# Kernel optimization log

Measured on AMD Instinct MI355X. Metric: run time of the kernel, lower is better.

Reference implementation:

```python
import jax, jax.numpy as jnp
import numpy as np

NEG_SLOPE = 0.2  # PyG GATConv LeakyReLU slope
N_NODES = 50000
N_EDGES = 800000
F_IN, HID, HEADS, N_CLS = 166, 64, 8, 2


def setup_inputs() -> dict:
    key = jax.random.key(0)
    ks = jax.random.split(key, 16)
    s = 0.1
    return {
        "x": jax.random.normal(ks[0], (N_NODES, F_IN), jnp.float32),
        "edge_index": jax.random.randint(ks[1], (2, N_EDGES), 0, N_NODES, jnp.int64),
        "W1": jax.random.normal(ks[2], (F_IN, HEADS * HID), jnp.float32) * s,
        "a_src1": jax.random.normal(ks[3], (HEADS, HID), jnp.float32) * s,
        "a_dst1": jax.random.normal(ks[4], (HEADS, HID), jnp.float32) * s,
        "b1": jnp.zeros((HEADS * HID,), jnp.float32),
        # conv_final: 512 -> 64, 1 head, mean (concat=False)
        "W2": jax.random.normal(ks[5], (HEADS * HID, HID), jnp.float32) * s,
        "a_src2": jax.random.normal(ks[6], (1, HID), jnp.float32) * s,
        "a_dst2": jax.random.normal(ks[7], (1, HID), jnp.float32) * s,
        "b2": jnp.zeros((HID,), jnp.float32),
        # classifier MLP 64 -> 64 -> 2
        "Wc1": jax.random.normal(ks[8], (HID, HID), jnp.float32) * s,
        "bc1": jnp.zeros((HID,), jnp.float32),
        "Wc2": jax.random.normal(ks[9], (HID, N_CLS), jnp.float32) * s,
        "bc2": jnp.zeros((N_CLS,), jnp.float32),
    }


def gat_layer(x, src, dst, W, a_src, a_dst, b, concat):
    """PyG-style GATConv (eval mode, self-loops already in src/dst)."""
    N = x.shape[0]
    H, C = a_src.shape
    xp = (x @ W).reshape(N, H, C)                 # [N,H,C] projected features
    al_src = jnp.sum(xp * a_src, axis=-1)         # [N,H]
    al_dst = jnp.sum(xp * a_dst, axis=-1)         # [N,H]
    e = jax.nn.leaky_relu(al_src[src] + al_dst[dst], NEG_SLOPE)  # [E,H]
    # segment softmax over incoming edges of each target node
    m = jax.ops.segment_max(e, dst, num_segments=N)
    ex = jnp.exp(e - m[dst])
    denom = jax.ops.segment_sum(ex, dst, num_segments=N)
    alpha = ex / denom[dst]                       # [E,H]
    out = jax.ops.segment_sum(alpha[:, :, None] * xp[src], dst, num_segments=N)  # [N,H,C]
    out = out.reshape(N, H * C) if concat else out.mean(axis=1)
    return out + b


def reference(x, edge_index, W1, a_src1, a_dst1, b1, W2, a_src2, a_dst2, b2, Wc1, bc1, Wc2, bc2):
    N = x.shape[0]
    loops = jnp.arange(N, dtype=edge_index.dtype)
    src = jnp.concatenate([edge_index[0], loops])  # add self-loops (PyG default)
    dst = jnp.concatenate([edge_index[1], loops])
    h = jax.nn.elu(gat_layer(x, src, dst, W1, a_src1, a_dst1, b1, concat=True))
    h = gat_layer(h, src, dst, W2, a_src2, a_dst2, b2, concat=False)
    h = jax.nn.relu(h @ Wc1 + bc1)
    return h @ Wc2 + bc2
```

## Files before the change

kernel.cpp:

```cpp
#include <hip/hip_runtime.h>

#define NN   50000
#define E0   800000
#define ET   850000
#define FIN  166
#define KP1  192
#define HID  64
#define NH   8
#define F1   512
#define SCHUNK 52
#define DEGPAD (1024*SCHUNK)

typedef __attribute__((ext_vector_type(8))) short short8;
typedef __attribute__((ext_vector_type(4))) float f32x4;
typedef __attribute__((ext_vector_type(4))) int int4v;
typedef unsigned short ush;

__device__ __forceinline__ float bf2f(unsigned short u){
  unsigned int x = ((unsigned int)u) << 16;
  return __builtin_bit_cast(float, x);
}
__device__ __forceinline__ unsigned short f2bf(float f){
  unsigned int x = __builtin_bit_cast(unsigned int, f);
  x += 0x7FFFu + ((x >> 16) & 1u);
  return (unsigned short)(x >> 16);
}

__global__ __launch_bounds__(256) void k_prep_all(const float* __restrict__ x,
                                                  const float* __restrict__ W1,
                                                  const float* __restrict__ W2,
                                                  const int* __restrict__ ei,
                                                  ush* __restrict__ xpad,
                                                  ush* __restrict__ W1t,
                                                  ush* __restrict__ W2t,
                                                  int* __restrict__ deg){
  const int T0 = NN*KP1;
  const int T1 = T0 + 512*KP1;
  const int T2 = T1 + HID*F1;
  const int T3 = T2 + ET;
  int i = blockIdx.x*256 + threadIdx.x;
  if (i >= T3) return;
  if (i < T0){
    int n = i / KP1, k = i % KP1;
    xpad[i] = f2bf(k < FIN ? x[(size_t)n*FIN + k] : 0.f);
  } else if (i < T1){
    int j = i - T0; int col = j / KP1, k = j % KP1;
    W1t[j] = f2bf(k < FIN ? W1[(size_t)k*512 + col] : 0.f);
  } else if (i < T2){
    int j = i - T1; int col = j / F1, k = j % F1;
    W2t[j] = f2bf(W2[(size_t)k*HID + col]);
  } else {
    int e = i - T2;
    int dst = (e < E0) ? ei[E0 + e] : (e - E0);
    atomicAdd(&deg[dst], 1);
  }
}

__global__ __launch_bounds__(1024) void k_scan(const int* __restrict__ deg,
                                               int* __restrict__ offs){
  __shared__ int sums[1024];
  int t = threadIdx.x;
  int base = t * SCHUNK;
  int4v v[13];
  int loc = 0;
  #pragma unroll
  for (int c = 0; c < 13; c++){
    v[c] = *(const int4v*)(deg + base + c*4);
    loc += v[c].x + v[c].y + v[c].z + v[c].w;
  }
  sums[t] = loc; __syncthreads();
  for (int off = 1; off < 1024; off <<= 1){
    int s = (t >= off) ? sums[t - off] : 0;
    __syncthreads();
    sums[t] += s;
    __syncthreads();
  }
  int run = sums[t] - loc;
  #pragma unroll
  for (int c = 0; c < 13; c++){
    int i0 = base + c*4;
    if (i0 + 0 < NN) offs[i0 + 0] = run;  run += v[c].x;
    if (i0 + 1 < NN) offs[i0 + 1] = run;  run += v[c].y;
    if (i0 + 2 < NN) offs[i0 + 2] = run;  run += v[c].z;
    if (i0 + 3 < NN) offs[i0 + 3] = run;  run += v[c].w;
  }
  if (t == 1023) offs[NN] = sums[1023];
}

__global__ __launch_bounds__(256) void k_scatter(const int* __restrict__ ei,
                                                 const int* __restrict__ offs,
                                                 int* __restrict__ cur,
                                                 int* __restrict__ esrc){
  for (int e = blockIdx.x*256 + threadIdx.x; e < ET; e += gridDim.x*256){
    int src, dst;
    if (e < E0){ src = ei[e]; dst = ei[E0 + e]; }
    else       { src = e - E0; dst = src; }
    int pos = offs[dst] + atomicAdd(&cur[dst], 1);
    esrc[pos] = src;
  }
}

__global__ __launch_bounds__(256) void k_gemm1(const ush* __restrict__ xpad,
                                               const ush* __restrict__ W1t,
                                               const float* __restrict__ a_s,
                                               const float* __restrict__ a_d,
                                               ush* __restrict__ xp1,
                                               float* __restrict__ als,
                                               float* __restrict__ ald){
  __shared__ ush As[128][40];
  __shared__ ush Bs[128][40];
  const int m0 = blockIdx.x*128, n0 = blockIdx.y*128;
  const int t = threadIdx.x, wid = t>>6, l = t&63;
  const int wr = wid>>1, wc = wid&1;
  const int lr = l&15, ksl = (l>>4)*8;
  const int srow = t>>1, sc = (t&1)*16;

  f32x4 acc[4][4];
  #pragma unroll
  for (int m = 0; m < 4; m++)
    #pragma unroll
    for (int n = 0; n < 4; n++)
      #pragma unroll
      for (int j = 0; j < 4; j++) acc[m][n][j] = 0.f;

  const int gr = m0 + srow;
  const ush* Ap = xpad + (size_t)gr*KP1 + sc;
  const ush* Bp = W1t + (size_t)(n0 + srow)*KP1 + sc;

  for (int s = 0; s < 6; s++){
    const int kk = s*32;
    short8 a0, a1;
    #pragma unroll
    for (int j = 0; j < 8; j++){ a0[j] = 0; a1[j] = 0; }
    if (gr < NN){ a0 = *(const short8*)(Ap + kk); a1 = *(const short8*)(Ap + kk + 8); }
    short8 b0 = *(const short8*)(Bp + kk);
    short8 b1 = *(const short8*)(Bp + kk + 8);
    *(short8*)&As[srow][sc]   = a0;
    *(short8*)&As[srow][sc+8] = a1;
    *(short8*)&Bs[srow][sc]   = b0;
    *(short8*)&Bs[srow][sc+8] = b1;
    __syncthreads();
    short8 af[4], bfr[4];
    #pragma unroll
    for (int m = 0; m < 4; m++) af[m]  = *(const short8*)&As[wr*64 + m*16 + lr][ksl];
    #pragma unroll
    for (int n = 0; n < 4; n++) bfr[n] = *(const short8*)&Bs[wc*64 + n*16 + lr][ksl];
    #pragma unroll
    for (int m = 0; m < 4; m++)
      #pragma unroll
      for (int n = 0; n < 4; n++)
        acc[m][n] = __builtin_amdgcn_mfma_f32_16x16x32_bf16(af[m], bfr[n], acc[m][n], 0, 0, 0);
    __syncthreads();
  }

  #pragma unroll
  for (int m = 0; m < 4; m++)
    #pragma unroll
    for (int n = 0; n < 4; n++)
      #pragma unroll
      for (int j = 0; j < 4; j++){
        int row = m0 + wr*64 + m*16 + (l>>4)*4 + j;
        int col = n0 + wc*64 + n*16 + lr;
        if (row < NN) xp1[(size_t)row*F1 + col] = f2bf(acc[m][n][j]);
      }

  const int head = blockIdx.y*2 + wc;
  float asv[4], adv[4];
  #pragma unroll
  for (int n = 0; n < 4; n++){
    asv[n] = a_s[head*64 + n*16 + lr];
    adv[n] = a_d[head*64 + n*16 + lr];
  }
  #pragma unroll
  for (int m = 0; m < 4; m++)
    #pragma unroll
    for (int j = 0; j < 4; j++){
      float ps = 0.f, pd = 0.f;
      #pragma unroll
      for (int n = 0; n < 4; n++){
        ps = fmaf(acc[m][n][j], asv[n], ps);
        pd = fmaf(acc[m][n][j], adv[n], pd);
      }
      #pragma unroll
      for (int o = 1; o < 16; o <<= 1){
        ps += __shfl_xor(ps, o, 64);
        pd += __shfl_xor(pd, o, 64);
      }
      if (lr == 0){
        int row = m0 + wr*64 + m*16 + (l>>4)*4 + j;
        if (row < NN){
          als[(size_t)row*NH + head] = fminf(fmaxf(ps, -30.f), 30.f);
          ald[(size_t)row*NH + head] = fminf(fmaxf(pd, -30.f), 30.f);
        }
      }
    }
}

__global__ __launch_bounds__(256) void k_gemm2(const ush* __restrict__ h1,
                                               const ush* __restrict__ W2t,
                                               const float* __restrict__ a_s,
                                               const float* __restrict__ a_d,
                                               ush* __restrict__ xp2,
                                               float* __restrict__ als,
                                               float* __restrict__ ald){
  __shared__ ush As[128][40];
  __shared__ ush Bs[64][40];
  const int m0 = blockIdx.x*128;
  const int t = threadIdx.x, wid = t>>6, l = t&63;
  const int lr = l&15, ksl = (l>>4)*8;
  const int srow = t>>1, sc = (t&1)*16;

  f32x4 acc[2][4];
  #pragma unroll
  for (int m = 0; m < 2; m++)
    #pragma unroll
    for (int n = 0; n < 4; n++)
      #pragma unroll
      for (int j = 0; j < 4; j++) acc[m][n][j] = 0.f;

  const int gr = m0 + srow;
  const ush* Ap = h1 + (size_t)gr*F1 + sc;
  const ush* Bp = W2t + (size_t)srow*F1 + sc;

  for (int s = 0; s < 16; s++){
    const int kk = s*32;
    short8 a0, a1;
    #pragma unroll
    for (int j = 0; j < 8; j++){ a0[j] = 0; a1[j] = 0; }
    if (gr < NN){ a0 = *(const short8*)(Ap + kk); a1 = *(const short8*)(Ap + kk + 8); }
    *(short8*)&As[srow][sc]   = a0;
    *(short8*)&As[srow][sc+8] = a1;
    if (t < 128){
      short8 b0 = *(const short8*)(Bp + kk);
      short8 b1 = *(const short8*)(Bp + kk + 8);
      *(short8*)&Bs[srow][sc]   = b0;
      *(short8*)&Bs[srow][sc+8] = b1;
    }
    __syncthreads();
    short8 af[2], bfr[4];
    #pragma unroll
    for (int m = 0; m < 2; m++) af[m]  = *(const short8*)&As[wid*32 + m*16 + lr][ksl];
    #pragma unroll
    for (int n = 0; n < 4; n++) bfr[n] = *(const short8*)&Bs[n*16 + lr][ksl];
    #pragma unroll
    for (int m = 0; m < 2; m++)
      #pragma unroll
      for (int n = 0; n < 4; n++)
        acc[m][n] = __builtin_amdgcn_mfma_f32_16x16x32_bf16(af[m], bfr[n], acc[m][n], 0, 0, 0);
    __syncthreads();
  }

  #pragma unroll
  for (int m = 0; m < 2; m++)
    #pragma unroll
    for (int n = 0; n < 4; n++)
      #pragma unroll
      for (int j = 0; j < 4; j++){
        int row = m0 + wid*32 + m*16 + (l>>4)*4 + j;
        int col = n*16 + lr;
        if (row < NN) xp2[(size_t)row*HID + col] = f2bf(acc[m][n][j]);
      }

  float asv[4], adv[4];
  #pragma unroll
  for (int n = 0; n < 4; n++){
    asv[n] = a_s[n*16 + lr];
    adv[n] = a_d[n*16 + lr];
  }
  #pragma unroll
  for (int m = 0; m < 2; m++)
    #pragma unroll
    for (int j = 0; j < 4; j++){
      float ps = 0.f, pd = 0.f;
      #pragma unroll
      for (int n = 0; n < 4; n++){
        ps = fmaf(acc[m][n][j], asv[n], ps);
        pd = fmaf(acc[m][n][j], adv[n], pd);
      }
      #pragma unroll
      for (int o = 1; o < 16; o <<= 1){
        ps += __shfl_xor(ps, o, 64);
        pd += __shfl_xor(pd, o, 64);
      }
      if (lr == 0){
        int row = m0 + wid*32 + m*16 + (l>>4)*4 + j;
        if (row < NN){
          als[row] = fminf(fmaxf(ps, -30.f), 30.f);
          ald[row] = fminf(fmaxf(pd, -30.f), 30.f);
        }
      }
    }
}

__global__ __launch_bounds__(256) void k_agg1(const int* __restrict__ offs,
                                              const int* __restrict__ esrc,
                                              const ush* __restrict__ xp1,
                                              const float* __restrict__ als,
                                              const float* __restrict__ ald,
                                              const float* __restrict__ b1,
                                              ush* __restrict__ h1){
  int w = (blockIdx.x*256 + threadIdx.x) >> 6;
  int l = threadIdx.x & 63;
  if (w >= NN) return;
  int h = l >> 3;
  int f0 = l * 8;
  float ad = ald[w*NH + h];
  int s0 = offs[w], s1 = offs[w+1];
  float accA[8], accB[8];
  #pragma unroll
  for (int j = 0; j < 8; j++){ accA[j] = 0.f; accB[j] = 0.f; }
  float den = 0.f;

  for (int base = s0; base < s1; base += 64){
    int cnt = min(64, s1 - base);
    int myE = (base + l < s1) ? esrc[base + l] : 0;
    int j = 0;
    for (; j + 4 <= cnt; j += 4){
      int sA = __shfl(myE, j,   64);
      int sB = __shfl(myE, j+1, 64);
      int sC = __shfl(myE, j+2, 64);
      int sD = __shfl(myE, j+3, 64);
      float eA = als[sA*NH + h] + ad;
      float eB = als[sB*NH + h] + ad;
      float eC = als[sC*NH + h] + ad;
      float eD = als[sD*NH + h] + ad;
      eA = fmaxf(eA, 0.2f*eA); eB = fmaxf(eB, 0.2f*eB);
      eC = fmaxf(eC, 0.2f*eC); eD = fmaxf(eD, 0.2f*eD);
      float wA = __expf(eA), wB = __expf(eB), wC = __expf(eC), wD = __expf(eD);
      short8 vA = *(const short8*)(xp1 + (size_t)sA*F1 + f0);
      short8 vB = *(const short8*)(xp1 + (size_t)sB*F1 + f0);
      short8 vC = *(const short8*)(xp1 + (size_t)sC*F1 + f0);
      short8 vD = *(const short8*)(xp1 + (size_t)sD*F1 + f0);
      den += (wA + wB) + (wC + wD);
      #pragma unroll
      for (int jj = 0; jj < 8; jj++){
        accA[jj] = fmaf(wA, bf2f((ush)vA[jj]), accA[jj]);
        accB[jj] = fmaf(wB, bf2f((ush)vB[jj]), accB[jj]);
        accA[jj] = fmaf(wC, bf2f((ush)vC[jj]), accA[jj]);
        accB[jj] = fmaf(wD, bf2f((ush)vD[jj]), accB[jj]);
      }
    }
    for (; j < cnt; j++){
      int sA = __shfl(myE, j, 64);
      float eA = als[sA*NH + h] + ad;
      eA = fmaxf(eA, 0.2f*eA);
      float wA = __expf(eA);
      short8 vA = *(const short8*)(xp1 + (size_t)sA*F1 + f0);
      den += wA;
      #pragma unroll
      for (int jj = 0; jj < 8; jj++)
        accA[jj] = fmaf(wA, bf2f((ush)vA[jj]), accA[jj]);
    }
  }
  float inv = 1.f / den;
  #pragma unroll
  for (int jj = 0; jj < 8; jj++){
    float o = (accA[jj] + accB[jj])*inv + b1[f0 + jj];
    o = o > 0.f ? o : expm1f(o);
    h1[(size_t)w*F1 + f0 + jj] = f2bf(o);
  }
}

__global__ __launch_bounds__(256) void k_agg2(const int* __restrict__ offs,
                                              const int* __restrict__ esrc,
                                              const ush* __restrict__ xp2,
                                              const float* __restrict__ als,
                                              const float* __restrict__ ald,
                                              const float* __restrict__ b2,
                                              const float* __restrict__ Wc1,
                                              const float* __restrict__ bc1,
                                              const float* __restrict__ Wc2,
                                              const float* __restrict__ bc2,
                                              float* __restrict__ out){
  int w = (blockIdx.x*256 + threadIdx.x) >> 6;
  int l = threadIdx.x & 63;
  if (w >= NN) return;
  float ad = ald[w];
  int s0 = offs[w], s1 = offs[w+1];
  float accA = 0.f, accB = 0.f, den = 0.f;

  for (int base = s0; base < s1; base += 64){
    int cnt = min(64, s1 - base);
    int myE = (base + l < s1) ? esrc[base + l] : 0;
    int j = 0;
    for (; j + 4 <= cnt; j += 4){
      int sA = __shfl(myE, j,   64);
      int sB = __shfl(myE, j+1, 64);
      int sC = __shfl(myE, j+2, 64);
      int sD = __shfl(myE, j+3, 64);
      float eA = als[sA] + ad, eB = als[sB] + ad, eC = als[sC] + ad, eD = als[sD] + ad;
      eA = fmaxf(eA, 0.2f*eA); eB = fmaxf(eB, 0.2f*eB);
      eC = fmaxf(eC, 0.2f*eC); eD = fmaxf(eD, 0.2f*eD);
      float wA = __expf(eA), wB = __expf(eB), wC = __expf(eC), wD = __expf(eD);
      float xA = bf2f(xp2[(size_t)sA*HID + l]);
      float xB = bf2f(xp2[(size_t)sB*HID + l]);
      float xC = bf2f(xp2[(size_t)sC*HID + l]);
      float xD = bf2f(xp2[(size_t)sD*HID + l]);
      den += (wA + wB) + (wC + wD);
      accA = fmaf(wA, xA, accA); accB = fmaf(wB, xB, accB);
      accA = fmaf(wC, xC, accA); accB = fmaf(wD, xD, accB);
    }
    for (; j < cnt; j++){
      int sA = __shfl(myE, j, 64);
      float eA = als[sA] + ad;
      eA = fmaxf(eA, 0.2f*eA);
      float wA = __expf(eA);
      den += wA;
      accA = fmaf(wA, bf2f(xp2[(size_t)sA*HID + l]), accA);
    }
  }
  float h2 = (accA + accB) / den + b2[l];
  float r = 0.f;
  #pragma unroll
  for (int k = 0; k < 64; k++){
    float hk = __shfl(h2, k, 64);
    r = fmaf(hk, Wc1[k*HID + l], r);
  }
  r += bc1[l];
  r = fmaxf(r, 0.f);
  float p0 = r * Wc2[l*2 + 0];
  float p1 = r * Wc2[l*2 + 1];
  #pragma unroll
  for (int o = 1; o < 64; o <<= 1){
    p0 += __shfl_xor(p0, o, 64);
    p1 += __shfl_xor(p1, o, 64);
  }
  if (l == 0){
    out[(size_t)w*2 + 0] = p0 + bc2[0];
    out[(size_t)w*2 + 1] = p1 + bc2[1];
  }
}

extern "C" void kernel_launch(void* const* d_in, const int* in_sizes, int n_in,
                              void* d_out, int out_size, void* d_ws, size_t ws_size,
                              hipStream_t stream){
  const float* x   = (const float*)d_in[0];
  const int*   ei  = (const int*)  d_in[1];
  const float* W1  = (const float*)d_in[2];
  const float* as1 = (const float*)d_in[3];
  const float* ad1 = (const float*)d_in[4];
  const float* b1  = (const float*)d_in[5];
  const float* W2  = (const float*)d_in[6];
  const float* as2 = (const float*)d_in[7];
  const float* ad2 = (const float*)d_in[8];
  const float* b2  = (const float*)d_in[9];
  const float* Wc1 = (const float*)d_in[10];
  const float* bc1 = (const float*)d_in[11];
  const float* Wc2 = (const float*)d_in[12];
  const float* bc2 = (const float*)d_in[13];
  float* out = (float*)d_out;

  char* p = (char*)d_ws; size_t off = 0;
  auto alloc = [&](size_t b){ void* r = p + off; off = (off + b + 255) & ~(size_t)255; return r; };
  ush* xpad = (ush*)alloc((size_t)NN*KP1*2);
  ush* W1t  = (ush*)alloc((size_t)512*KP1*2);
  ush* W2t  = (ush*)alloc((size_t)HID*F1*2);
  ush* xp1  = (ush*)alloc((size_t)NN*F1*2);
  ush* h1   = (ush*)alloc((size_t)NN*F1*2);
  ush* xp2  = (ush*)alloc((size_t)NN*HID*2);
  float* als1 = (float*)alloc((size_t)NN*NH*4);
  float* ald1 = (float*)alloc((size_t)NN*NH*4);
  float* als2 = (float*)alloc((size_t)NN*4);
  float* ald2 = (float*)alloc((size_t)NN*4);
  int* deg  = (int*)alloc((size_t)DEGPAD*4);
  int* cur  = (int*)alloc((size_t)NN*4);
  int* offs = (int*)alloc((size_t)(NN+1)*4);
  int* esrc = (int*)alloc((size_t)ET*4);

  hipMemsetAsync(deg, 0, (size_t)DEGPAD*4, stream);
  hipMemsetAsync(cur, 0, (size_t)NN*4, stream);

  const int T3 = NN*KP1 + 512*KP1 + HID*F1 + ET;
  k_prep_all<<<(T3 + 255)/256, 256, 0, stream>>>(x, W1, W2, ei, xpad, W1t, W2t, deg);
  k_scan<<<1, 1024, 0, stream>>>(deg, offs);
  k_scatter<<<(ET + 255)/256, 256, 0, stream>>>(ei, offs, cur, esrc);

  k_gemm1<<<dim3(391, 4), 256, 0, stream>>>(xpad, W1t, as1, ad1, xp1, als1, ald1);
  k_agg1<<<12500, 256, 0, stream>>>(offs, esrc, xp1, als1, ald1, b1, h1);

  k_gemm2<<<391, 256, 0, stream>>>(h1, W2t, as2, ad2, xp2, als2, ald2);
  k_agg2<<<12500, 256, 0, stream>>>(offs, esrc, xp2, als2, ald2, b2, Wc1, bc1, Wc2, bc2, out);
}
```

Baseline: 394.0 us.

## Precompute per-edge attention weights in separate kernels before aggregation

Adds a destination array to the CSR scatter and two new edge-wise kernels that compute leaky-relu and exp attention weights per edge (and per head) into workspace buffers. The aggregation kernels then read these weights from contiguous CSR-ordered memory instead of gathering als by source and running exp inline. The change removes random als gathers and exp work from the gather-bound aggregation loops. In exchange it adds two kernel launches and extra global traffic, about 27 MB written and read for layer 1 weights, plus an edst array. It also splits the first aggregation into two half-node launches.

```diff
diff --git a/kernel.cpp b/kernel.cpp
--- a/kernel.cpp
+++ b/kernel.cpp
@@ -90,13 +90,15 @@
 __global__ __launch_bounds__(256) void k_scatter(const int* __restrict__ ei,
                                                  const int* __restrict__ offs,
                                                  int* __restrict__ cur,
-                                                 int* __restrict__ esrc){
+                                                 int* __restrict__ esrc,
+                                                 int* __restrict__ edst){
   for (int e = blockIdx.x*256 + threadIdx.x; e < ET; e += gridDim.x*256){
     int src, dst;
     if (e < E0){ src = ei[e]; dst = ei[E0 + e]; }
     else       { src = e - E0; dst = src; }
     int pos = offs[dst] + atomicAdd(&cur[dst], 1);
     esrc[pos] = src;
+    edst[pos] = dst;
   }
 }
 
@@ -292,19 +294,45 @@
     }
 }
 
+__global__ __launch_bounds__(256) void k_ew1(const int* __restrict__ esrc,
+                                             const int* __restrict__ edst,
+                                             const float* __restrict__ als,
+                                             const float* __restrict__ ald,
+                                             float* __restrict__ wt1){
+  int i = blockIdx.x*256 + threadIdx.x;
+  if (i >= ET*NH) return;
+  int pos = i >> 3, h = i & 7;
+  int src = esrc[pos], dst = edst[pos];
+  float v = als[src*NH + h] + ald[dst*NH + h];
+  v = fmaxf(v, 0.2f*v);
+  wt1[i] = __expf(v);
+}
+
+__global__ __launch_bounds__(256) void k_ew2(const int* __restrict__ esrc,
+                                             const int* __restrict__ edst,
+                                             const float* __restrict__ als,
+                                             const float* __restrict__ ald,
+                                             float* __restrict__ wt2){
+  int pos = blockIdx.x*256 + threadIdx.x;
+  if (pos >= ET) return;
+  float v = als[esrc[pos]] + ald[edst[pos]];
+  v = fmaxf(v, 0.2f*v);
+  wt2[pos] = __expf(v);
+}
+
 __global__ __launch_bounds__(256) void k_agg1(const int* __restrict__ offs,
                                               const int* __restrict__ esrc,
                                               const ush* __restrict__ xp1,
-                                              const float* __restrict__ als,
-                                              const float* __restrict__ ald,
+                                              const float* __restrict__ wt1,
                                               const float* __restrict__ b1,
-                                              ush* __restrict__ h1){
+                                              ush* __restrict__ h1,
+                                              int nodeBase, int nodeCnt){
   int w = (blockIdx.x*256 + threadIdx.x) >> 6;
   int l = threadIdx.x & 63;
-  if (w >= NN) return;
+  if (w >= nodeCnt) return;
+  w += nodeBase;
   int h = l >> 3;
   int f0 = l * 8;
-  float ad = ald[w*NH + h];
   int s0 = offs[w], s1 = offs[w+1];
   float accA[8], accB[8];
   #pragma unroll
@@ -320,13 +348,10 @@
       int sB = __shfl(myE, j+1, 64);
       int sC = __shfl(myE, j+2, 64);
       int sD = __shfl(myE, j+3, 64);
-      float eA = als[sA*NH + h] + ad;
-      float eB = als[sB*NH + h] + ad;
-      float eC = als[sC*NH + h] + ad;
-      float eD = als[sD*NH + h] + ad;
-      eA = fmaxf(eA, 0.2f*eA); eB = fmaxf(eB, 0.2f*eB);
-      eC = fmaxf(eC, 0.2f*eC); eD = fmaxf(eD, 0.2f*eD);
-      float wA = __expf(eA), wB = __expf(eB), wC = __expf(eC), wD = __expf(eD);
+      float wA = wt1[(size_t)(base+j  )*NH + h];
+      float wB = wt1[(size_t)(base+j+1)*NH + h];
+      float wC = wt1[(size_t)(base+j+2)*NH + h];
+      float wD = wt1[(size_t)(base+j+3)*NH + h];
       short8 vA = *(const short8*)(xp1 + (size_t)sA*F1 + f0);
       short8 vB = *(const short8*)(xp1 + (size_t)sB*F1 + f0);
       short8 vC = *(const short8*)(xp1 + (size_t)sC*F1 + f0);
@@ -342,9 +367,7 @@
     }
     for (; j < cnt; j++){
       int sA = __shfl(myE, j, 64);
-      float eA = als[sA*NH + h] + ad;
-      eA = fmaxf(eA, 0.2f*eA);
-      float wA = __expf(eA);
+      float wA = wt1[(size_t)(base+j)*NH + h];
       short8 vA = *(const short8*)(xp1 + (size_t)sA*F1 + f0);
       den += wA;
       #pragma unroll
@@ -364,8 +387,7 @@
 __global__ __launch_bounds__(256) void k_agg2(const int* __restrict__ offs,
                                               const int* __restrict__ esrc,
                                               const ush* __restrict__ xp2,
-                                              const float* __restrict__ als,
-                                              const float* __restrict__ ald,
+                                              const float* __restrict__ wt2,
                                               const float* __restrict__ b2,
                                               const float* __restrict__ Wc1,
                                               const float* __restrict__ bc1,
@@ -375,7 +397,6 @@
   int w = (blockIdx.x*256 + threadIdx.x) >> 6;
   int l = threadIdx.x & 63;
   if (w >= NN) return;
-  float ad = ald[w];
   int s0 = offs[w], s1 = offs[w+1];
   float accA = 0.f, accB = 0.f, den = 0.f;
 
@@ -388,10 +409,7 @@
       int sB = __shfl(myE, j+1, 64);
       int sC = __shfl(myE, j+2, 64);
       int sD = __shfl(myE, j+3, 64);
-      float eA = als[sA] + ad, eB = als[sB] + ad, eC = als[sC] + ad, eD = als[sD] + ad;
-      eA = fmaxf(eA, 0.2f*eA); eB = fmaxf(eB, 0.2f*eB);
-      eC = fmaxf(eC, 0.2f*eC); eD = fmaxf(eD, 0.2f*eD);
-      float wA = __expf(eA), wB = __expf(eB), wC = __expf(eC), wD = __expf(eD);
+      float wA = wt2[base+j], wB = wt2[base+j+1], wC = wt2[base+j+2], wD = wt2[base+j+3];
       float xA = bf2f(xp2[(size_t)sA*HID + l]);
       float xB = bf2f(xp2[(size_t)sB*HID + l]);
       float xC = bf2f(xp2[(size_t)sC*HID + l]);
@@ -402,9 +420,7 @@
     }
     for (; j < cnt; j++){
       int sA = __shfl(myE, j, 64);
-      float eA = als[sA] + ad;
-      eA = fmaxf(eA, 0.2f*eA);
-      float wA = __expf(eA);
+      float wA = wt2[base+j];
       den += wA;
       accA = fmaf(wA, bf2f(xp2[(size_t)sA*HID + l]), accA);
     }
@@ -462,10 +478,13 @@
   float* ald1 = (float*)alloc((size_t)NN*NH*4);
   float* als2 = (float*)alloc((size_t)NN*4);
   float* ald2 = (float*)alloc((size_t)NN*4);
+  float* wt1  = (float*)alloc((size_t)ET*NH*4);
+  float* wt2  = (float*)alloc((size_t)ET*4);
   int* deg  = (int*)alloc((size_t)DEGPAD*4);
   int* cur  = (int*)alloc((size_t)NN*4);
   int* offs = (int*)alloc((size_t)(NN+1)*4);
   int* esrc = (int*)alloc((size_t)ET*4);
+  int* edst = (int*)alloc((size_t)ET*4);
 
   hipMemsetAsync(deg, 0, (size_t)DEGPAD*4, stream);
   hipMemsetAsync(cur, 0, (size_t)NN*4, stream);
@@ -473,11 +492,14 @@
   const int T3 = NN*KP1 + 512*KP1 + HID*F1 + ET;
   k_prep_all<<<(T3 + 255)/256, 256, 0, stream>>>(x, W1, W2, ei, xpad, W1t, W2t, deg);
   k_scan<<<1, 1024, 0, stream>>>(deg, offs);
-  k_scatter<<<(ET + 255)/256, 256, 0, stream>>>(ei, offs, cur, esrc);
+  k_scatter<<<(ET + 255)/256, 256, 0, stream>>>(ei, offs, cur, esrc, edst);
 
   k_gemm1<<<dim3(391, 4), 256, 0, stream>>>(xpad, W1t, as1, ad1, xp1, als1, ald1);
-  k_agg1<<<12500, 256, 0, stream>>>(offs, esrc, xp1, als1, ald1, b1, h1);
+  k_ew1<<<(ET*NH + 255)/256, 256, 0, stream>>>(esrc, edst, als1, ald1, wt1);
+  k_agg1<<<6250, 256, 0, stream>>>(offs, esrc, xp1, wt1, b1, h1, 0,     25000);
+  k_agg1<<<6250, 256, 0, stream>>>(offs, esrc, xp1, wt1, b1, h1, 25000, 25000);
 
   k_gemm2<<<391, 256, 0, stream>>>(h1, W2t, as2, ad2, xp2, als2, ald2);
-  k_agg2<<<12500, 256, 0, stream>>>(offs, esrc, xp2, als2, ald2, b2, Wc1, bc1, Wc2, bc2, out);
-}
+  k_ew2<<<(ET + 255)/256, 256, 0, stream>>>(esrc, edst, als2, ald2, wt2);
+  k_agg2<<<12500, 256, 0, stream>>>(offs, esrc, xp2, wt2, b2, Wc1, bc1, Wc2, bc2, out);
+}
```

Result: slower. 430.6 us (+9.3%).

## Split layer-1 aggregation into feature slices with 16 edges per wave

Applied to the files above, without the earlier changes.

The layer-1 aggregation kernel is restructured so each wave handles one 32-feature slice of one node instead of all 512 features. Lanes in groups of four cover the slice, and 16 edges are processed in parallel, with a cross-lane reduction at the end. Blocks are ordered in two phases by slice so that the xp1 columns being gathered at any moment fit in cache. The cost is 16x more waves, repeated reads of offsets, edge lists and attention logits, and extra shuffle reductions.

```diff
diff --git a/kernel.cpp b/kernel.cpp
--- a/kernel.cpp
+++ b/kernel.cpp
@@ -10,6 +10,8 @@
 #define F1   512
 #define SCHUNK 52
 #define DEGPAD (1024*SCHUNK)
+#define GRPS 12500
+#define BLKS_PER_PHASE (GRPS*8)
 
 typedef __attribute__((ext_vector_type(8))) short short8;
 typedef __attribute__((ext_vector_type(4))) float f32x4;
@@ -299,65 +301,62 @@
                                               const float* __restrict__ ald,
                                               const float* __restrict__ b1,
                                               ush* __restrict__ h1){
-  int w = (blockIdx.x*256 + threadIdx.x) >> 6;
+  int bid = blockIdx.x;
+  int phase = bid / BLKS_PER_PHASE;
+  int r = bid - phase*BLKS_PER_PHASE;
+  int slice = (r & 7) + (phase << 3);
+  int node = (r >> 3)*4 + (threadIdx.x >> 6);
   int l = threadIdx.x & 63;
-  if (w >= NN) return;
-  int h = l >> 3;
-  int f0 = l * 8;
-  float ad = ald[w*NH + h];
-  int s0 = offs[w], s1 = offs[w+1];
-  float accA[8], accB[8];
-  #pragma unroll
-  for (int j = 0; j < 8; j++){ accA[j] = 0.f; accB[j] = 0.f; }
+  int head = slice >> 1;
+  int f0 = slice*32 + (l & 3)*8;
+  float ad = ald[node*NH + head];
+  int s0 = offs[node], s1 = offs[node+1];
+
+  float acc[8];
+  #pragma unroll
+  for (int j = 0; j < 8; j++) acc[j] = 0.f;
   float den = 0.f;
+  int g = l >> 2;
 
   for (int base = s0; base < s1; base += 64){
-    int cnt = min(64, s1 - base);
     int myE = (base + l < s1) ? esrc[base + l] : 0;
-    int j = 0;
-    for (; j + 4 <= cnt; j += 4){
-      int sA = __shfl(myE, j,   64);
-      int sB = __shfl(myE, j+1, 64);
-      int sC = __shfl(myE, j+2, 64);
-      int sD = __shfl(myE, j+3, 64);
-      float eA = als[sA*NH + h] + ad;
-      float eB = als[sB*NH + h] + ad;
-      float eC = als[sC*NH + h] + ad;
-      float eD = als[sD*NH + h] + ad;
-      eA = fmaxf(eA, 0.2f*eA); eB = fmaxf(eB, 0.2f*eB);
-      eC = fmaxf(eC, 0.2f*eC); eD = fmaxf(eD, 0.2f*eD);
-      float wA = __expf(eA), wB = __expf(eB), wC = __expf(eC), wD = __expf(eD);
-      short8 vA = *(const short8*)(xp1 + (size_t)sA*F1 + f0);
-      short8 vB = *(const short8*)(xp1 + (size_t)sB*F1 + f0);
-      short8 vC = *(const short8*)(xp1 + (size_t)sC*F1 + f0);
-      short8 vD = *(const short8*)(xp1 + (size_t)sD*F1 + f0);
-      den += (wA + wB) + (wC + wD);
-      #pragma unroll
-      for (int jj = 0; jj < 8; jj++){
-        accA[jj] = fmaf(wA, bf2f((ush)vA[jj]), accA[jj]);
-        accB[jj] = fmaf(wB, bf2f((ush)vB[jj]), accB[jj]);
-        accA[jj] = fmaf(wC, bf2f((ush)vC[jj]), accA[jj]);
-        accB[jj] = fmaf(wD, bf2f((ush)vD[jj]), accB[jj]);
-      }
-    }
-    for (; j < cnt; j++){
-      int sA = __shfl(myE, j, 64);
-      float eA = als[sA*NH + h] + ad;
-      eA = fmaxf(eA, 0.2f*eA);
-      float wA = __expf(eA);
-      short8 vA = *(const short8*)(xp1 + (size_t)sA*F1 + f0);
-      den += wA;
-      #pragma unroll
-      for (int jj = 0; jj < 8; jj++)
-        accA[jj] = fmaf(wA, bf2f((ush)vA[jj]), accA[jj]);
-    }
-  }
-  float inv = 1.f / den;
-  #pragma unroll
-  for (int jj = 0; jj < 8; jj++){
-    float o = (accA[jj] + accB[jj])*inv + b1[f0 + jj];
-    o = o > 0.f ? o : expm1f(o);
-    h1[(size_t)w*F1 + f0 + jj] = f2bf(o);
+    int nsub = min(64, s1 - base);
+    for (int sub = 0; sub*16 < nsub; sub++){
+      int aSrc = __shfl(myE, sub*16 + (l & 15), 64);
+      float w_ = 0.f;
+      if (l < 16 && base + sub*16 + l < s1){
+        float e_ = als[aSrc*NH + head] + ad;
+        e_ = fmaxf(e_, 0.2f*e_);
+        w_ = __expf(e_);
+      }
+      int eidx = base + sub*16 + g;
+      int gSrc = __shfl(myE, sub*16 + g, 64);
+      float wt = __shfl(w_, g, 64);
+      if (eidx < s1){
+        short8 v = *(const short8*)(xp1 + (size_t)gSrc*F1 + f0);
+        den += wt;
+        #pragma unroll
+        for (int j = 0; j < 8; j++)
+          acc[j] = fmaf(wt, bf2f((ush)v[j]), acc[j]);
+      }
+    }
+  }
+  #pragma unroll
+  for (int o = 4; o < 64; o <<= 1){
+    den += __shfl_xor(den, o, 64);
+    #pragma unroll
+    for (int j = 0; j < 8; j++) acc[j] += __shfl_xor(acc[j], o, 64);
+  }
+  if (l < 4){
+    float inv = 1.f / den;
+    short8 ov;
+    #pragma unroll
+    for (int j = 0; j < 8; j++){
+      float o = acc[j]*inv + b1[f0 + j];
+      o = o > 0.f ? o : expm1f(o);
+      ov[j] = (short)f2bf(o);
+    }
+    *(short8*)(h1 + (size_t)node*F1 + f0) = ov;
   }
 }
 
@@ -476,7 +475,7 @@
   k_scatter<<<(ET + 255)/256, 256, 0, stream>>>(ei, offs, cur, esrc);
 
   k_gemm1<<<dim3(391, 4), 256, 0, stream>>>(xpad, W1t, as1, ad1, xp1, als1, ald1);
-  k_agg1<<<12500, 256, 0, stream>>>(offs, esrc, xp1, als1, ald1, b1, h1);
+  k_agg1<<<2*BLKS_PER_PHASE, 256, 0, stream>>>(offs, esrc, xp1, als1, ald1, b1, h1);
 
   k_gemm2<<<391, 256, 0, stream>>>(h1, W2t, as2, ad2, xp2, als2, ald2);
   k_agg2<<<12500, 256, 0, stream>>>(offs, esrc, xp2, als2, ald2, b2, Wc1, bc1, Wc2, bc2, out);
```

Result: slower. 839.2 us (+113.0%).

## Precompute layer-2 edge weights in a separate kernel and unroll agg2 by eight

Applied to the files above, without the earlier changes.

Adds an edge-parallel kernel that computes exp(leaky_relu(als[src]+ald[dst])) once per edge for layer 2. To support it, the scatter step now also records each edge's destination. The aggregation kernel then reads these weights coalesced and broadcasts them by shuffle, and its inner loop is unrolled from four to eight edges for more memory-level parallelism. This removes the redundant per-lane dependent gathers of als and the exp calls in agg2. The cost is an extra launch, extra edst and wt2 traffic (about 7 MB), and the extra write in scatter.

```diff
diff --git a/kernel.cpp b/kernel.cpp
--- a/kernel.cpp
+++ b/kernel.cpp
@@ -90,13 +90,15 @@
 __global__ __launch_bounds__(256) void k_scatter(const int* __restrict__ ei,
                                                  const int* __restrict__ offs,
                                                  int* __restrict__ cur,
-                                                 int* __restrict__ esrc){
+                                                 int* __restrict__ esrc,
+                                                 int* __restrict__ edst){
   for (int e = blockIdx.x*256 + threadIdx.x; e < ET; e += gridDim.x*256){
     int src, dst;
     if (e < E0){ src = ei[e]; dst = ei[E0 + e]; }
     else       { src = e - E0; dst = src; }
     int pos = offs[dst] + atomicAdd(&cur[dst], 1);
     esrc[pos] = src;
+    edst[pos] = dst;
   }
 }
 
@@ -290,6 +292,18 @@
         }
       }
     }
+}
+
+__global__ __launch_bounds__(256) void k_ew2(const int* __restrict__ esrc,
+                                             const int* __restrict__ edst,
+                                             const float* __restrict__ als,
+                                             const float* __restrict__ ald,
+                                             float* __restrict__ wt2){
+  int pos = blockIdx.x*256 + threadIdx.x;
+  if (pos >= ET) return;
+  float v = als[esrc[pos]] + ald[edst[pos]];
+  v = fmaxf(v, 0.2f*v);
+  wt2[pos] = __expf(v);
 }
 
 __global__ __launch_bounds__(256) void k_agg1(const int* __restrict__ offs,
@@ -364,8 +378,7 @@
 __global__ __launch_bounds__(256) void k_agg2(const int* __restrict__ offs,
                                               const int* __restrict__ esrc,
                                               const ush* __restrict__ xp2,
-                                              const float* __restrict__ als,
-                                              const float* __restrict__ ald,
+                                              const float* __restrict__ wt2,
                                               const float* __restrict__ b2,
                                               const float* __restrict__ Wc1,
                                               const float* __restrict__ bc1,
@@ -375,36 +388,41 @@
   int w = (blockIdx.x*256 + threadIdx.x) >> 6;
   int l = threadIdx.x & 63;
   if (w >= NN) return;
-  float ad = ald[w];
   int s0 = offs[w], s1 = offs[w+1];
   float accA = 0.f, accB = 0.f, den = 0.f;
 
   for (int base = s0; base < s1; base += 64){
     int cnt = min(64, s1 - base);
-    int myE = (base + l < s1) ? esrc[base + l] : 0;
+    bool ok = (base + l < s1);
+    int   myE = ok ? esrc[base + l] : 0;
+    float myW = ok ? wt2[base + l] : 0.f;
     int j = 0;
-    for (; j + 4 <= cnt; j += 4){
-      int sA = __shfl(myE, j,   64);
-      int sB = __shfl(myE, j+1, 64);
-      int sC = __shfl(myE, j+2, 64);
-      int sD = __shfl(myE, j+3, 64);
-      float eA = als[sA] + ad, eB = als[sB] + ad, eC = als[sC] + ad, eD = als[sD] + ad;
-      eA = fmaxf(eA, 0.2f*eA); eB = fmaxf(eB, 0.2f*eB);
-      eC = fmaxf(eC, 0.2f*eC); eD = fmaxf(eD, 0.2f*eD);
-      float wA = __expf(eA), wB = __expf(eB), wC = __expf(eC), wD = __expf(eD);
+    for (; j + 8 <= cnt; j += 8){
+      int sA = __shfl(myE, j,   64), sB = __shfl(myE, j+1, 64);
+      int sC = __shfl(myE, j+2, 64), sD = __shfl(myE, j+3, 64);
+      int sE = __shfl(myE, j+4, 64), sF = __shfl(myE, j+5, 64);
+      int sG = __shfl(myE, j+6, 64), sH = __shfl(myE, j+7, 64);
+      float wA = __shfl(myW, j,   64), wB = __shfl(myW, j+1, 64);
+      float wC = __shfl(myW, j+2, 64), wD = __shfl(myW, j+3, 64);
+      float wE = __shfl(myW, j+4, 64), wF = __shfl(myW, j+5, 64);
+      float wG = __shfl(myW, j+6, 64), wH = __shfl(myW, j+7, 64);
       float xA = bf2f(xp2[(size_t)sA*HID + l]);
       float xB = bf2f(xp2[(size_t)sB*HID + l]);
       float xC = bf2f(xp2[(size_t)sC*HID + l]);
       float xD = bf2f(xp2[(size_t)sD*HID + l]);
-      den += (wA + wB) + (wC + wD);
+      float xE = bf2f(xp2[(size_t)sE*HID + l]);
+      float xF = bf2f(xp2[(size_t)sF*HID + l]);
+      float xG = bf2f(xp2[(size_t)sG*HID + l]);
+      float xH = bf2f(xp2[(size_t)sH*HID + l]);
+      den += ((wA + wB) + (wC + wD)) + ((wE + wF) + (wG + wH));
       accA = fmaf(wA, xA, accA); accB = fmaf(wB, xB, accB);
       accA = fmaf(wC, xC, accA); accB = fmaf(wD, xD, accB);
+      accA = fmaf(wE, xE, accA); accB = fmaf(wF, xF, accB);
+      accA = fmaf(wG, xG, accA); accB = fmaf(wH, xH, accB);
     }
     for (; j < cnt; j++){
       int sA = __shfl(myE, j, 64);
-      float eA = als[sA] + ad;
-      eA = fmaxf(eA, 0.2f*eA);
-      float wA = __expf(eA);
+      float wA = __shfl(myW, j, 64);
       den += wA;
       accA = fmaf(wA, bf2f(xp2[(size_t)sA*HID + l]), accA);
     }
@@ -462,10 +480,12 @@
   float* ald1 = (float*)alloc((size_t)NN*NH*4);
   float* als2 = (float*)alloc((size_t)NN*4);
   float* ald2 = (float*)alloc((size_t)NN*4);
+  float* wt2  = (float*)alloc((size_t)ET*4);
   int* deg  = (int*)alloc((size_t)DEGPAD*4);
   int* cur  = (int*)alloc((size_t)NN*4);
   int* offs = (int*)alloc((size_t)(NN+1)*4);
   int* esrc = (int*)alloc((size_t)ET*4);
+  int* edst = (int*)alloc((size_t)ET*4);
 
   hipMemsetAsync(deg, 0, (size_t)DEGPAD*4, stream);
   hipMemsetAsync(cur, 0, (size_t)NN*4, stream);
@@ -473,11 +493,12 @@
   const int T3 = NN*KP1 + 512*KP1 + HID*F1 + ET;
   k_prep_all<<<(T3 + 255)/256, 256, 0, stream>>>(x, W1, W2, ei, xpad, W1t, W2t, deg);
   k_scan<<<1, 1024, 0, stream>>>(deg, offs);
-  k_scatter<<<(ET + 255)/256, 256, 0, stream>>>(ei, offs, cur, esrc);
+  k_scatter<<<(ET + 255)/256, 256, 0, stream>>>(ei, offs, cur, esrc, edst);
 
   k_gemm1<<<dim3(391, 4), 256, 0, stream>>>(xpad, W1t, as1, ad1, xp1, als1, ald1);
   k_agg1<<<12500, 256, 0, stream>>>(offs, esrc, xp1, als1, ald1, b1, h1);
 
   k_gemm2<<<391, 256, 0, stream>>>(h1, W2t, as2, ad2, xp2, als2, ald2);
-  k_agg2<<<12500, 256, 0, stream>>>(offs, esrc, xp2, als2, ald2, b2, Wc1, bc1, Wc2, bc2, out);
-}
+  k_ew2<<<(ET + 255)/256, 256, 0, stream>>>(esrc, edst, als2, ald2, wt2);
+  k_agg2<<<12500, 256, 0, stream>>>(offs, esrc, xp2, wt2, b2, Wc1, bc1, Wc2, bc2, out);
+}
```

After: 418.6 us. 6.2% more time.
